# Performance work log

Measured on AMD Instinct MI355X. Metric: run time of the kernel, lower is better.

Reference implementation:

```python
import jax, jax.numpy as jnp
import numpy as np

B, S, H, A, V = 128, 128, 1024, 1024, 50000
NEG = -1e11  # mask value used by the original for zero scores (padded positions)


def setup_inputs() -> dict:
    key = jax.random.key(0)
    ks = jax.random.split(key, 10)
    b_ih = jnp.zeros((4 * H,), jnp.float32).at[H:2 * H].set(1.0)  # forget_bias
    b_hh = jnp.zeros((4 * H,), jnp.float32).at[H:2 * H].set(1.0)
    return {
        "input": jax.random.randint(ks[0], (B,), 0, V),
        "prev_h": jax.random.normal(ks[1], (B, H), jnp.float32),
        "prev_c": jax.random.normal(ks[2], (B, H), jnp.float32),
        "encoder_output": jax.random.normal(ks[3], (B, S, H), jnp.float32),
        "emb": jax.random.normal(ks[4], (V, H), jnp.float32) * 0.02,
        "W_ih": jax.random.normal(ks[5], (4 * H, H), jnp.float32) * 0.02,
        "W_hh": jax.random.normal(ks[6], (4 * H, H), jnp.float32) * 0.02,
        "b_ih": b_ih,
        "b_hh": b_hh,
        "W_out": jax.random.normal(ks[7], (A, 2 * H), jnp.float32) * 0.02,
        "b_out": jnp.zeros((A,), jnp.float32),
        "W_out2": jax.random.normal(ks[8], (V, A), jnp.float32) * 0.02,
        "b_out2": jnp.zeros((V,), jnp.float32),
    }


def reference(input, prev_h, prev_c, encoder_output, emb, W_ih, W_hh, b_ih, b_hh,
              W_out, b_out, W_out2, b_out2):
    # embedding lookup (dropout p=0 -> identity)
    x = emb[input]  # [B, H]
    # LSTMCell, PyTorch gate order (i, f, g, o)
    gates = x @ W_ih.T + b_ih + prev_h @ W_hh.T + b_hh  # [B, 4H]
    i, f, g, o = jnp.split(gates, 4, axis=-1)
    c = jax.nn.sigmoid(f) * prev_c + jax.nn.sigmoid(i) * jnp.tanh(g)
    h = jax.nn.sigmoid(o) * jnp.tanh(c)
    # dot attention over (padded) encoder outputs
    scores = jnp.einsum("bsh,bh->bs", encoder_output, h)  # [B, S]
    scores = jnp.where(scores == 0, NEG, scores)          # mask padded rows
    attn = jax.nn.softmax(scores, axis=1)
    context = jnp.einsum("bsh,bs->bh", encoder_output, attn)  # [B, H]
    # MLP decode
    attention_vector = jnp.tanh(jnp.concatenate([context, h], axis=-1) @ W_out.T + b_out)
    logits = attention_vector @ W_out2.T + b_out2  # [B, V]
    output = jax.nn.log_softmax(logits, axis=1)
    return output, h, c
```

## Files before the change

### kernel.cpp

```cpp
#include <hip/hip_runtime.h>
#include <hip/hip_bf16.h>
#include <math.h>

#define Bn 128
#define Sn 128
#define Hn 1024
#define Vn 50000

using short8  = __attribute__((ext_vector_type(8))) short;
using floatx4 = __attribute__((ext_vector_type(4))) float;

__device__ __forceinline__ unsigned short f2bf_bits(float f) {
  union { __hip_bfloat16 h; unsigned short u; } cv;
  cv.h = __float2bfloat16(f);
  return cv.u;
}
__device__ __forceinline__ float bf_bits2f(unsigned short u) {
  union { __hip_bfloat16 h; unsigned short u; } cv;
  cv.u = u;
  return __bfloat162float(cv.h);
}
__device__ __forceinline__ short8 cvt8(float4 a, float4 b) {
  short8 r;
  r[0]=(short)f2bf_bits(a.x); r[1]=(short)f2bf_bits(a.y);
  r[2]=(short)f2bf_bits(a.z); r[3]=(short)f2bf_bits(a.w);
  r[4]=(short)f2bf_bits(b.x); r[5]=(short)f2bf_bits(b.y);
  r[6]=(short)f2bf_bits(b.z); r[7]=(short)f2bf_bits(b.w);
  return r;
}
__device__ __forceinline__ void split8(float4 a, float4 b, short8& hi, short8& lo) {
  float f[8] = {a.x,a.y,a.z,a.w,b.x,b.y,b.z,b.w};
#pragma unroll
  for (int i=0;i<8;++i) {
    unsigned short h = f2bf_bits(f[i]);
    hi[i] = (short)h;
    lo[i] = (short)f2bf_bits(f[i] - bf_bits2f(h));
  }
}
__device__ __forceinline__ floatx4 mfma16(short8 a, short8 b, floatx4 c) {
  return __builtin_amdgcn_mfma_f32_16x16x32_bf16(a, b, c, 0, 0, 0);
}

__global__ void __launch_bounds__(256) k1_pack(const int* __restrict__ inp,
    const float* __restrict__ prev_h, const float* __restrict__ emb,
    unsigned short* __restrict__ xh_hi, unsigned short* __restrict__ xh_lo) {
  int idx = blockIdx.x*256 + threadIdx.x;
  int b = idx >> 11, k = idx & 2047;
  if (k < 1024) {
    float v = emb[(size_t)inp[b]*Hn + k];
    xh_hi[idx] = f2bf_bits(v);
  } else {
    float v = prev_h[b*Hn + (k-1024)];
    unsigned short hi = f2bf_bits(v);
    xh_hi[idx] = hi;
    xh_lo[b*Hn + (k-1024)] = f2bf_bits(v - bf_bits2f(hi));
  }
}

__global__ void __launch_bounds__(64) k2_gates(
    const unsigned short* __restrict__ xh_hi, const unsigned short* __restrict__ xh_lo,
    const float* __restrict__ W_ih, const float* __restrict__ W_hh,
    const float* __restrict__ b_ih, const float* __restrict__ b_hh,
    float* __restrict__ gates) {
  int lane = threadIdx.x, l15 = lane & 15, quad = lane >> 4;
  int n = blockIdx.x*16 + l15;
  int mt = blockIdx.y;
  floatx4 acc = {0.f,0.f,0.f,0.f};

  for (int k0 = 0; k0 < 1024; k0 += 32) {
    int k = k0 + quad*8;
    const float* wp = W_ih + (size_t)n*Hn + k;
    float4 w0 = *(const float4*)wp;
    float4 w1 = *(const float4*)(wp+4);
    short8 bfrag = cvt8(w0,w1);
    short8 afrag = *(const short8*)(xh_hi + (mt*16 + l15)*2048 + k);
    acc = mfma16(afrag, bfrag, acc);
  }
  for (int k0 = 0; k0 < 1024; k0 += 32) {
    int k = k0 + quad*8;
    const float* wp = W_hh + (size_t)n*Hn + k;
    float4 w0 = *(const float4*)wp;
    float4 w1 = *(const float4*)(wp+4);
    short8 whi, wlo; split8(w0,w1,whi,wlo);
    short8 ahi = *(const short8*)(xh_hi + (mt*16 + l15)*2048 + 1024 + k);
    short8 alo = *(const short8*)(xh_lo + (mt*16 + l15)*1024 + k);
    acc = mfma16(ahi, whi, acc);
    acc = mfma16(alo, whi, acc);
    acc = mfma16(ahi, wlo, acc);
  }
  float bias = b_ih[n] + b_hh[n];
#pragma unroll
  for (int r=0;r<4;++r) {
    int m = mt*16 + quad*4 + r;
    gates[m*4096 + n] = acc[r] + bias;
  }
}

__global__ void __launch_bounds__(256) k3_lstm(const float* __restrict__ gates,
    const float* __restrict__ prev_c, float* __restrict__ out,
    float* __restrict__ h32, unsigned short* __restrict__ ctxh) {
  int idx = blockIdx.x*256 + threadIdx.x;
  int b = idx >> 10, k = idx & 1023;
  const float* g = gates + b*4096;
  float gi = g[k], gf = g[k+1024], gg = g[k+2048], go = g[k+3072];
  float si = 1.f/(1.f+expf(-gi));
  float sf = 1.f/(1.f+expf(-gf));
  float so = 1.f/(1.f+expf(-go));
  float c = sf*prev_c[idx] + si*tanhf(gg);
  float h = so*tanhf(c);
  out[6400000 + idx] = h;
  out[6531072 + idx] = c;
  h32[idx] = h;
  ctxh[b*2048 + 1024 + k] = f2bf_bits(h);
}

__global__ void __launch_bounds__(256) k4a_scores(const float* __restrict__ enc,
    const float* __restrict__ h32, float* __restrict__ scores) {
  int w = blockIdx.x*4 + (threadIdx.x>>6);
  int lane = threadIdx.x & 63;
  int b = w >> 7, s = w & 127;
  const float* e = enc + (size_t)(b*Sn + s)*Hn;
  const float* hp = h32 + b*Hn;
  float sum = 0.f;
#pragma unroll
  for (int j=0;j<4;++j) {
    int k = j*256 + lane*4;
    float4 ev = *(const float4*)(e+k);
    float4 hv = *(const float4*)(hp+k);
    sum += ev.x*hv.x + ev.y*hv.y + ev.z*hv.z + ev.w*hv.w;
  }
#pragma unroll
  for (int o=32;o>0;o>>=1) sum += __shfl_xor(sum, o, 64);
  if (lane==0) {
    if (sum == 0.f) sum = -1e11f;
    scores[b*Sn+s] = sum;
  }
}

__global__ void __launch_bounds__(256) k4b_ctx(const float* __restrict__ enc,
    const float* __restrict__ scores, unsigned short* __restrict__ ctxh) {
  __shared__ float sc[128];
  __shared__ float red[128];
  int tid = threadIdx.x, b = blockIdx.y;
  if (tid < 128) { float v = scores[b*Sn+tid]; sc[tid] = v; red[tid] = v; }
  __syncthreads();
  for (int st=64; st>0; st>>=1) {
    if (tid<st) red[tid] = fmaxf(red[tid], red[tid+st]);
    __syncthreads();
  }
  float mx = red[0];
  __syncthreads();
  if (tid<128) { float e = expf(sc[tid]-mx); sc[tid]=e; red[tid]=e; }
  __syncthreads();
  for (int st=64; st>0; st>>=1) {
    if (tid<st) red[tid] += red[tid+st];
    __syncthreads();
  }
  float inv = 1.0f/red[0];
  __syncthreads();
  if (tid<128) sc[tid] *= inv;
  __syncthreads();
  int hcol = blockIdx.x*256 + tid;
  const float* e = enc + (size_t)b*(Sn*Hn) + hcol;
  float acc = 0.f;
#pragma unroll 8
  for (int s2=0; s2<128; ++s2) acc += sc[s2]*e[(size_t)s2*Hn];
  ctxh[b*2048 + hcol] = f2bf_bits(acc);
}

__global__ void __launch_bounds__(64) k5_att(const unsigned short* __restrict__ ctxh,
    const float* __restrict__ W_out, const float* __restrict__ b_out,
    unsigned short* __restrict__ av) {
  int lane = threadIdx.x, l15 = lane&15, quad = lane>>4;
  int n = blockIdx.x*16 + l15;
  int mt = blockIdx.y;
  floatx4 acc = {0.f,0.f,0.f,0.f};
  for (int k0=0;k0<2048;k0+=32) {
    int k = k0 + quad*8;
    const float* wp = W_out + (size_t)n*2048 + k;
    float4 w0=*(const float4*)wp, w1=*(const float4*)(wp+4);
    short8 bfrag = cvt8(w0,w1);
    short8 afrag = *(const short8*)(ctxh + (mt*16 + l15)*2048 + k);
    acc = mfma16(afrag, bfrag, acc);
  }
  float bias = b_out[n];
#pragma unroll
  for (int r=0;r<4;++r) {
    int m = mt*16 + quad*4 + r;
    av[m*Hn + n] = f2bf_bits(tanhf(acc[r] + bias));
  }
}

__global__ void __launch_bounds__(256) k6a_logits(const unsigned short* __restrict__ av,
    const float* __restrict__ W2, const float* __restrict__ b2,
    float* __restrict__ out) {
  __shared__ unsigned short lA[2][128*40];
  __shared__ unsigned short lB[2][64*40];
  int tid = threadIdx.x;
  int wave = tid>>6, lane = tid&63, l15 = lane&15, quad = lane>>4;
  int tileN = blockIdx.x*64;

  int arow = tid>>2, apart = tid&3;
  int brow = tid>>3, bpart = tid&7;

  uint4 aR0, aR1; float4 wR0, wR1;

  auto gload = [&](int k0) {
    aR0 = *(const uint4*)(av + (size_t)arow*Hn + k0 + apart*8);
    aR1 = *(const uint4*)(av + (size_t)(arow+64)*Hn + k0 + apart*8);
    int r0 = tileN + brow;      if (r0 > Vn-1) r0 = Vn-1;
    int r1 = tileN + brow + 32; if (r1 > Vn-1) r1 = Vn-1;
    wR0 = *(const float4*)(W2 + (size_t)r0*Hn + k0 + bpart*4);
    wR1 = *(const float4*)(W2 + (size_t)r1*Hn + k0 + bpart*4);
  };
  auto lstore = [&](int buf) {
    *(uint4*)(&lA[buf][arow*40 + apart*8])      = aR0;
    *(uint4*)(&lA[buf][(arow+64)*40 + apart*8]) = aR1;
    ushort4 p0, p1;
    p0.x=f2bf_bits(wR0.x); p0.y=f2bf_bits(wR0.y); p0.z=f2bf_bits(wR0.z); p0.w=f2bf_bits(wR0.w);
    p1.x=f2bf_bits(wR1.x); p1.y=f2bf_bits(wR1.y); p1.z=f2bf_bits(wR1.z); p1.w=f2bf_bits(wR1.w);
    *(ushort4*)(&lB[buf][brow*40 + bpart*4])      = p0;
    *(ushort4*)(&lB[buf][(brow+32)*40 + bpart*4]) = p1;
  };

  floatx4 z = {0.f,0.f,0.f,0.f};
  floatx4 acc[8];
#pragma unroll
  for (int t=0;t<8;++t) acc[t]=z;

  gload(0);
  lstore(0);
  __syncthreads();

  for (int kc=0; kc<32; ++kc) {
    int cur = kc&1;
    if (kc<31) gload((kc+1)*32);
    short8 bfrag = *(const short8*)(&lB[cur][(wave*16+l15)*40 + quad*8]);
    short8 af[8];
#pragma unroll
    for (int t=0;t<8;++t)
      af[t] = *(const short8*)(&lA[cur][(t*16+l15)*40 + quad*8]);
#pragma unroll
    for (int t=0;t<8;++t)
      acc[t] = mfma16(af[t], bfrag, acc[t]);
    if (kc<31) {
      __syncthreads();
      lstore(1-cur);
      __syncthreads();
    }
  }

  int n = tileN + wave*16 + l15;
  if (n < Vn) {
    float bias = b2[n];
#pragma unroll
    for (int t=0;t<8;++t)
#pragma unroll
      for (int r=0;r<4;++r) {
        int m = t*16 + quad*4 + r;
        out[(size_t)m*Vn + n] = acc[t][r] + bias;
      }
  }
}

__global__ void __launch_bounds__(256) k6b1_lse(const float* __restrict__ logits,
    float* __restrict__ pm, float* __restrict__ ps) {
  int b = blockIdx.y, c = blockIdx.x, tid = threadIdx.x;
  int v0 = c*6250, v1 = v0 + 6250;
  const float* row = logits + (size_t)b*Vn;
  float m = -3.4e38f, s = 0.f;
  for (int v = v0 + tid; v < v1; v += 256) {
    float x = row[v];
    float nm = fmaxf(m, x);
    s = s*expf(m-nm) + expf(x-nm);
    m = nm;
  }
  __shared__ float sm[256], ss[256];
  sm[tid]=m; ss[tid]=s;
  __syncthreads();
  for (int st=128; st>0; st>>=1) {
    if (tid<st) {
      float m1=sm[tid], m2=sm[tid+st];
      float nm=fmaxf(m1,m2);
      ss[tid]=ss[tid]*expf(m1-nm)+ss[tid+st]*expf(m2-nm);
      sm[tid]=nm;
    }
    __syncthreads();
  }
  if (tid==0) { pm[b*8+c]=sm[0]; ps[b*8+c]=ss[0]; }
}

__global__ void __launch_bounds__(128) k6b2_lse(const float* __restrict__ pm,
    const float* __restrict__ ps, float* __restrict__ lse) {
  int b = threadIdx.x;
  float m = -3.4e38f, s = 0.f;
#pragma unroll
  for (int c=0;c<8;++c) {
    float m2 = pm[b*8+c], s2 = ps[b*8+c];
    float nm = fmaxf(m, m2);
    s = s*expf(m-nm) + s2*expf(m2-nm);
    m = nm;
  }
  lse[b] = m + logf(s);
}

__global__ void __launch_bounds__(256) k6c_sub(float* __restrict__ out,
    const float* __restrict__ lse) {
  int f = blockIdx.x*256 + threadIdx.x;
  if (f >= 12500) return;
  int b = blockIdx.y;
  float l = lse[b];
  float4* p = (float4*)(out + (size_t)b*Vn) + f;
  float4 v = *p;
  v.x -= l; v.y -= l; v.z -= l; v.w -= l;
  *p = v;
}

extern "C" void kernel_launch(void* const* d_in, const int* in_sizes, int n_in,
                              void* d_out, int out_size, void* d_ws, size_t ws_size,
                              hipStream_t stream) {
  const int*   inp    = (const int*)d_in[0];
  const float* prev_h = (const float*)d_in[1];
  const float* prev_c = (const float*)d_in[2];
  const float* enc    = (const float*)d_in[3];
  const float* emb    = (const float*)d_in[4];
  const float* W_ih   = (const float*)d_in[5];
  const float* W_hh   = (const float*)d_in[6];
  const float* b_ih   = (const float*)d_in[7];
  const float* b_hh   = (const float*)d_in[8];
  const float* W_out  = (const float*)d_in[9];
  const float* b_out  = (const float*)d_in[10];
  const float* W_out2 = (const float*)d_in[11];
  const float* b_out2 = (const float*)d_in[12];
  float* out = (float*)d_out;
  char* ws = (char*)d_ws;

  unsigned short* xh_hi = (unsigned short*)(ws + 0);
  unsigned short* xh_lo = (unsigned short*)(ws + 524288);
  float* gates          = (float*)(ws + 786432);
  float* h32            = (float*)(ws + 2883584);
  float* scores         = (float*)(ws + 3407872);
  unsigned short* ctxh  = (unsigned short*)(ws + 3473408);
  unsigned short* av    = (unsigned short*)(ws + 3997696);
  float* lse            = (float*)(ws + 4259840);
  float* pm             = (float*)(ws + 4260352);
  float* ps             = (float*)(ws + 4264448);

  k1_pack   <<<1024, 256, 0, stream>>>(inp, prev_h, emb, xh_hi, xh_lo);
  k2_gates  <<<dim3(256,8), 64, 0, stream>>>(xh_hi, xh_lo, W_ih, W_hh, b_ih, b_hh, gates);
  k3_lstm   <<<512, 256, 0, stream>>>(gates, prev_c, out, h32, ctxh);
  k4a_scores<<<4096, 256, 0, stream>>>(enc, h32, scores);
  k4b_ctx   <<<dim3(4,128), 256, 0, stream>>>(enc, scores, ctxh);
  k5_att    <<<dim3(64,8), 64, 0, stream>>>(ctxh, W_out, b_out, av);
  k6a_logits<<<782, 256, 0, stream>>>(av, W_out2, b_out2, out);
  k6b1_lse  <<<dim3(8,128), 256, 0, stream>>>(out, pm, ps);
  k6b2_lse  <<<1, 128, 0, stream>>>(pm, ps, lse);
  k6c_sub   <<<dim3(49,128), 256, 0, stream>>>(out, lse);
}
```

Before: 628.7 us.

## Fuse LSTM gates with cell update and fold log-softmax partials into logits GEMM

Merges the gate GEMM and the LSTM pointwise kernel, so each block computes all four gate tiles for a 16x16 output patch, combines them in shared memory and writes h and c directly. This removes the gates round-trip through global memory. The logits GEMM epilogue now computes per-tile row max and sum-exp with lane shuffles, so the separate pass that re-read the 128x50000 logits for LSE is gone. One barrier is dropped from the double-buffered K loop. Finalising LSE and subtracting it are merged into one kernel with one block per row, which is less parallel than the previous subtract grid.

```diff
diff --git a/kernel.cpp b/kernel.cpp
--- a/kernel.cpp
+++ b/kernel.cpp
@@ -6,6 +6,7 @@
 #define Sn 128
 #define Hn 1024
 #define Vn 50000
+#define NT 782
 
 using short8  = __attribute__((ext_vector_type(8))) short;
 using floatx4 = __attribute__((ext_vector_type(4))) float;
@@ -57,61 +58,56 @@
   }
 }
 
-__global__ void __launch_bounds__(64) k2_gates(
+__global__ void __launch_bounds__(256) k2b_gates_lstm(
     const unsigned short* __restrict__ xh_hi, const unsigned short* __restrict__ xh_lo,
     const float* __restrict__ W_ih, const float* __restrict__ W_hh,
     const float* __restrict__ b_ih, const float* __restrict__ b_hh,
-    float* __restrict__ gates) {
-  int lane = threadIdx.x, l15 = lane & 15, quad = lane >> 4;
-  int n = blockIdx.x*16 + l15;
-  int mt = blockIdx.y;
-  floatx4 acc = {0.f,0.f,0.f,0.f};
-
-  for (int k0 = 0; k0 < 1024; k0 += 32) {
-    int k = k0 + quad*8;
-    const float* wp = W_ih + (size_t)n*Hn + k;
-    float4 w0 = *(const float4*)wp;
-    float4 w1 = *(const float4*)(wp+4);
-    short8 bfrag = cvt8(w0,w1);
-    short8 afrag = *(const short8*)(xh_hi + (mt*16 + l15)*2048 + k);
-    acc = mfma16(afrag, bfrag, acc);
-  }
-  for (int k0 = 0; k0 < 1024; k0 += 32) {
-    int k = k0 + quad*8;
-    const float* wp = W_hh + (size_t)n*Hn + k;
-    float4 w0 = *(const float4*)wp;
-    float4 w1 = *(const float4*)(wp+4);
-    short8 whi, wlo; split8(w0,w1,whi,wlo);
-    short8 ahi = *(const short8*)(xh_hi + (mt*16 + l15)*2048 + 1024 + k);
-    short8 alo = *(const short8*)(xh_lo + (mt*16 + l15)*1024 + k);
-    acc = mfma16(ahi, whi, acc);
-    acc = mfma16(alo, whi, acc);
-    acc = mfma16(ahi, wlo, acc);
-  }
-  float bias = b_ih[n] + b_hh[n];
-#pragma unroll
-  for (int r=0;r<4;++r) {
-    int m = mt*16 + quad*4 + r;
-    gates[m*4096 + n] = acc[r] + bias;
-  }
-}
-
-__global__ void __launch_bounds__(256) k3_lstm(const float* __restrict__ gates,
     const float* __restrict__ prev_c, float* __restrict__ out,
     float* __restrict__ h32, unsigned short* __restrict__ ctxh) {
-  int idx = blockIdx.x*256 + threadIdx.x;
-  int b = idx >> 10, k = idx & 1023;
-  const float* g = gates + b*4096;
-  float gi = g[k], gf = g[k+1024], gg = g[k+2048], go = g[k+3072];
-  float si = 1.f/(1.f+expf(-gi));
-  float sf = 1.f/(1.f+expf(-gf));
-  float so = 1.f/(1.f+expf(-go));
-  float c = sf*prev_c[idx] + si*tanhf(gg);
-  float h = so*tanhf(c);
-  out[6400000 + idx] = h;
-  out[6531072 + idx] = c;
-  h32[idx] = h;
-  ctxh[b*2048 + 1024 + k] = f2bf_bits(h);
+  __shared__ float g4[4][16][16];
+  int tid = threadIdx.x;
+  int g = tid>>6, lane = tid&63, l15 = lane&15, quad = lane>>4;
+  int n16 = blockIdx.x*16;
+  int mt  = blockIdx.y;
+  int ncol = g*1024 + n16 + l15;
+  floatx4 acc = {0.f,0.f,0.f,0.f};
+
+  for (int k0=0;k0<1024;k0+=32) {
+    int k = k0 + quad*8;
+    const float* wp = W_ih + (size_t)ncol*Hn + k;
+    float4 w0=*(const float4*)wp, w1=*(const float4*)(wp+4);
+    short8 bfrag = cvt8(w0,w1);
+    short8 afrag = *(const short8*)(xh_hi + (mt*16+l15)*2048 + k);
+    acc = mfma16(afrag,bfrag,acc);
+  }
+  for (int k0=0;k0<1024;k0+=32) {
+    int k = k0 + quad*8;
+    const float* wp = W_hh + (size_t)ncol*Hn + k;
+    float4 w0=*(const float4*)wp, w1=*(const float4*)(wp+4);
+    short8 whi, wlo; split8(w0,w1,whi,wlo);
+    short8 ahi = *(const short8*)(xh_hi + (mt*16+l15)*2048 + 1024 + k);
+    short8 alo = *(const short8*)(xh_lo + (mt*16+l15)*1024 + k);
+    acc = mfma16(ahi,whi,acc);
+    acc = mfma16(alo,whi,acc);
+    acc = mfma16(ahi,wlo,acc);
+  }
+  float bias = b_ih[ncol] + b_hh[ncol];
+#pragma unroll
+  for (int r=0;r<4;++r)
+    g4[g][quad*4+r][l15] = acc[r] + bias;
+  __syncthreads();
+
+  int r = tid>>4, c = tid&15;
+  int m = mt*16 + r;
+  int k = n16 + c;
+  float gi=g4[0][r][c], gf=g4[1][r][c], gg=g4[2][r][c], go=g4[3][r][c];
+  float si=1.f/(1.f+expf(-gi)), sf=1.f/(1.f+expf(-gf)), so=1.f/(1.f+expf(-go));
+  float cc = sf*prev_c[m*Hn+k] + si*tanhf(gg);
+  float h  = so*tanhf(cc);
+  out[6400000 + m*Hn + k] = h;
+  out[6531072 + m*Hn + k] = cc;
+  h32[m*Hn+k] = h;
+  ctxh[m*2048 + 1024 + k] = f2bf_bits(h);
 }
 
 __global__ void __launch_bounds__(256) k4a_scores(const float* __restrict__ enc,
@@ -193,16 +189,17 @@
 
 __global__ void __launch_bounds__(256) k6a_logits(const unsigned short* __restrict__ av,
     const float* __restrict__ W2, const float* __restrict__ b2,
-    float* __restrict__ out) {
+    float* __restrict__ out, float2* __restrict__ pmps) {
   __shared__ unsigned short lA[2][128*40];
   __shared__ unsigned short lB[2][64*40];
+  __shared__ float smax[4][128];
+  __shared__ float ssum[4][128];
   int tid = threadIdx.x;
   int wave = tid>>6, lane = tid&63, l15 = lane&15, quad = lane>>4;
   int tileN = blockIdx.x*64;
 
   int arow = tid>>2, apart = tid&3;
   int brow = tid>>3, bpart = tid&7;
-
   uint4 aR0, aR1; float4 wR0, wR1;
 
   auto gload = [&](int k0) {
@@ -233,49 +230,66 @@
   __syncthreads();
 
   for (int kc=0; kc<32; ++kc) {
-    int cur = kc&1;
+    int p = kc&1;
     if (kc<31) gload((kc+1)*32);
-    short8 bfrag = *(const short8*)(&lB[cur][(wave*16+l15)*40 + quad*8]);
-    short8 af[8];
-#pragma unroll
-    for (int t=0;t<8;++t)
-      af[t] = *(const short8*)(&lA[cur][(t*16+l15)*40 + quad*8]);
-#pragma unroll
-    for (int t=0;t<8;++t)
-      acc[t] = mfma16(af[t], bfrag, acc[t]);
-    if (kc<31) {
-      __syncthreads();
-      lstore(1-cur);
-      __syncthreads();
+    short8 bfrag = *(const short8*)(&lB[p][(wave*16+l15)*40 + quad*8]);
+#pragma unroll
+    for (int t=0;t<8;++t) {
+      short8 af = *(const short8*)(&lA[p][(t*16+l15)*40 + quad*8]);
+      acc[t] = mfma16(af, bfrag, acc[t]);
     }
+    if (kc<31) { lstore(1-p); __syncthreads(); }
   }
 
   int n = tileN + wave*16 + l15;
-  if (n < Vn) {
-    float bias = b2[n];
-#pragma unroll
-    for (int t=0;t<8;++t)
-#pragma unroll
-      for (int r=0;r<4;++r) {
-        int m = t*16 + quad*4 + r;
-        out[(size_t)m*Vn + n] = acc[t][r] + bias;
-      }
-  }
-}
-
-__global__ void __launch_bounds__(256) k6b1_lse(const float* __restrict__ logits,
-    float* __restrict__ pm, float* __restrict__ ps) {
-  int b = blockIdx.y, c = blockIdx.x, tid = threadIdx.x;
-  int v0 = c*6250, v1 = v0 + 6250;
-  const float* row = logits + (size_t)b*Vn;
+  bool valid = n < Vn;
+  float bias = valid ? b2[n] : 0.f;
+#pragma unroll
+  for (int t=0;t<8;++t) {
+#pragma unroll
+    for (int r=0;r<4;++r) {
+      float v = acc[t][r] + bias;
+      int m = t*16 + quad*4 + r;
+      if (valid) out[(size_t)m*Vn + n] = v;
+      float xv = valid ? v : -3.4e38f;
+      float mx = xv;
+      mx = fmaxf(mx, __shfl_xor(mx, 1));
+      mx = fmaxf(mx, __shfl_xor(mx, 2));
+      mx = fmaxf(mx, __shfl_xor(mx, 4));
+      mx = fmaxf(mx, __shfl_xor(mx, 8));
+      float e = expf(xv - mx);
+      e += __shfl_xor(e, 1);
+      e += __shfl_xor(e, 2);
+      e += __shfl_xor(e, 4);
+      e += __shfl_xor(e, 8);
+      if (l15 == 0) { smax[wave][m] = mx; ssum[wave][m] = e; }
+    }
+  }
+  __syncthreads();
+  if (tid < 128) {
+    float m = smax[0][tid], s = ssum[0][tid];
+#pragma unroll
+    for (int w=1;w<4;++w) {
+      float m2 = smax[w][tid], s2 = ssum[w][tid];
+      float nm = fmaxf(m, m2);
+      s = s*expf(m-nm) + s2*expf(m2-nm);
+      m = nm;
+    }
+    pmps[(size_t)tid*NT + blockIdx.x] = make_float2(m, s);
+  }
+}
+
+__global__ void __launch_bounds__(256) k6c_final(float* __restrict__ out,
+    const float2* __restrict__ pmps) {
+  __shared__ float sm[256], ss[256];
+  int b = blockIdx.x, tid = threadIdx.x;
   float m = -3.4e38f, s = 0.f;
-  for (int v = v0 + tid; v < v1; v += 256) {
-    float x = row[v];
-    float nm = fmaxf(m, x);
-    s = s*expf(m-nm) + expf(x-nm);
+  for (int i = tid; i < NT; i += 256) {
+    float2 v = pmps[(size_t)b*NT + i];
+    float nm = fmaxf(m, v.x);
+    s = s*expf(m-nm) + v.y*expf(v.x-nm);
     m = nm;
   }
-  __shared__ float sm[256], ss[256];
   sm[tid]=m; ss[tid]=s;
   __syncthreads();
   for (int st=128; st>0; st>>=1) {
@@ -287,33 +301,13 @@
     }
     __syncthreads();
   }
-  if (tid==0) { pm[b*8+c]=sm[0]; ps[b*8+c]=ss[0]; }
-}
-
-__global__ void __launch_bounds__(128) k6b2_lse(const float* __restrict__ pm,
-    const float* __restrict__ ps, float* __restrict__ lse) {
-  int b = threadIdx.x;
-  float m = -3.4e38f, s = 0.f;
-#pragma unroll
-  for (int c=0;c<8;++c) {
-    float m2 = pm[b*8+c], s2 = ps[b*8+c];
-    float nm = fmaxf(m, m2);
-    s = s*expf(m-nm) + s2*expf(m2-nm);
-    m = nm;
-  }
-  lse[b] = m + logf(s);
-}
-
-__global__ void __launch_bounds__(256) k6c_sub(float* __restrict__ out,
-    const float* __restrict__ lse) {
-  int f = blockIdx.x*256 + threadIdx.x;
-  if (f >= 12500) return;
-  int b = blockIdx.y;
-  float l = lse[b];
-  float4* p = (float4*)(out + (size_t)b*Vn) + f;
-  float4 v = *p;
-  v.x -= l; v.y -= l; v.z -= l; v.w -= l;
-  *p = v;
+  float lse = sm[0] + logf(ss[0]);
+  float4* row = (float4*)(out + (size_t)b*Vn);
+  for (int f = tid; f < 12500; f += 256) {
+    float4 v = row[f];
+    v.x-=lse; v.y-=lse; v.z-=lse; v.w-=lse;
+    row[f]=v;
+  }
 }
 
 extern "C" void kernel_launch(void* const* d_in, const int* in_sizes, int n_in,
@@ -337,23 +331,18 @@
 
   unsigned short* xh_hi = (unsigned short*)(ws + 0);
   unsigned short* xh_lo = (unsigned short*)(ws + 524288);
-  float* gates          = (float*)(ws + 786432);
-  float* h32            = (float*)(ws + 2883584);
-  float* scores         = (float*)(ws + 3407872);
-  unsigned short* ctxh  = (unsigned short*)(ws + 3473408);
-  unsigned short* av    = (unsigned short*)(ws + 3997696);
-  float* lse            = (float*)(ws + 4259840);
-  float* pm             = (float*)(ws + 4260352);
-  float* ps             = (float*)(ws + 4264448);
+  float* h32            = (float*)(ws + 786432);
+  float* scores         = (float*)(ws + 1310720);
+  unsigned short* ctxh  = (unsigned short*)(ws + 1376256);
+  unsigned short* av    = (unsigned short*)(ws + 1900544);
+  float2* pmps          = (float2*)(ws + 2162688);
 
   k1_pack   <<<1024, 256, 0, stream>>>(inp, prev_h, emb, xh_hi, xh_lo);
-  k2_gates  <<<dim3(256,8), 64, 0, stream>>>(xh_hi, xh_lo, W_ih, W_hh, b_ih, b_hh, gates);
-  k3_lstm   <<<512, 256, 0, stream>>>(gates, prev_c, out, h32, ctxh);
+  k2b_gates_lstm<<<dim3(64,8), 256, 0, stream>>>(xh_hi, xh_lo, W_ih, W_hh, b_ih, b_hh,
+                                                 prev_c, out, h32, ctxh);
   k4a_scores<<<4096, 256, 0, stream>>>(enc, h32, scores);
   k4b_ctx   <<<dim3(4,128), 256, 0, stream>>>(enc, scores, ctxh);
   k5_att    <<<dim3(64,8), 64, 0, stream>>>(ctxh, W_out, b_out, av);
-  k6a_logits<<<782, 256, 0, stream>>>(av, W_out2, b_out2, out);
-  k6b1_lse  <<<dim3(8,128), 256, 0, stream>>>(out, pm, ps);
-  k6b2_lse  <<<1, 128, 0, stream>>>(pm, ps, lse);
-  k6c_sub   <<<dim3(49,128), 256, 0, stream>>>(out, lse);
-}
+  k6a_logits<<<NT, 256, 0, stream>>>(av, W_out2, b_out2, out, pmps);
+  k6c_final <<<128, 256, 0, stream>>>(out, pmps);
+}
```

New measurement: 628.8 us. Within noise of the previous version (+0.0%).
